# Kernel optimization log

Measured on AMD Instinct MI355X. Metric: run time of the kernel, lower is better.

Reference implementation:

```python
import jax, jax.numpy as jnp
import numpy as np

B, L, D, H = 2, 2048, 1024, 16
DK = D // H


def setup_inputs() -> dict:
    key = jax.random.key(0)
    ks = jax.random.split(key, 11)
    s = 1.0 / np.sqrt(D)
    inp = {
        "context_sequence": jax.random.normal(ks[0], (B, L, D), jnp.float32),
        "value_sequence": jax.random.normal(ks[1], (B, L, D), jnp.float32),
        "mask": jnp.tril(jnp.ones((L, L), jnp.int32)),  # causal mask [L, L]
        "Wq": jax.random.normal(ks[2], (D, D), jnp.float32) * s,
        "bq": jax.random.normal(ks[3], (D,), jnp.float32) * s,
        "Wk": jax.random.normal(ks[4], (D, D), jnp.float32) * s,
        "bk": jax.random.normal(ks[5], (D,), jnp.float32) * s,
        "Wv": jax.random.normal(ks[6], (D, D), jnp.float32) * s,
        "bv": jax.random.normal(ks[7], (D,), jnp.float32) * s,
        "Wo": jax.random.normal(ks[8], (D, D), jnp.float32) * s,
        "bo": jax.random.normal(ks[9], (D,), jnp.float32) * s,
    }
    return inp


def reference(context_sequence, value_sequence, mask, Wq, bq, Wk, bk, Wv, bv, Wo, bo):
    orig_dtype = context_sequence.dtype
    # QKV projections; Q,K from context, V from value stream
    Q = (context_sequence @ Wq + bq).reshape(B, L, H, DK)
    K = (context_sequence @ Wk + bk).reshape(B, L, H, DK)
    V = (value_sequence @ Wv + bv).reshape(B, L, H, DK)
    # fp32 QK^T with 1/sqrt(d_k) scaling -> [B, H, L, L]
    scores = jnp.einsum("bqhd,bkhd->bhqk", Q.astype(jnp.float32), K.astype(jnp.float32)) / jnp.sqrt(
        jnp.asarray(DK, jnp.float32)
    )
    # dtype-dependent neg fill (fp32 -> -inf); causal rows always have >=1 valid entry
    neg_fill = jnp.asarray(-jnp.inf, jnp.float32)
    scores = jnp.where(mask[None, None, :, :] == 0, neg_fill, scores)
    scores = scores.astype(orig_dtype)
    attn = jax.nn.softmax(scores, axis=-1)
    # dropout is identity in eval mode
    out = jnp.einsum("bhqk,bkhd->bqhd", attn, V).reshape(B, L, D)
    return out @ Wo + bo
```

## Files before the change

### kernel.cpp

```cpp
#include <hip/hip_runtime.h>
#include <hip/hip_bf16.h>
#include <stdint.h>

#define B_   2
#define L_   2048
#define D_   1024
#define H_   16
#define DK_  64

typedef __attribute__((ext_vector_type(4))) float f32x4;
typedef __attribute__((ext_vector_type(8))) short short8;
typedef unsigned short ushort_t;

__device__ __forceinline__ ushort_t f2bf(float f) {
    union { float f; uint32_t u; } v; v.f = f;
    uint32_t r = v.u + 0x7FFFu + ((v.u >> 16) & 1u);
    return (ushort_t)(r >> 16);
}
__device__ __forceinline__ float bf2f(ushort_t u) {
    union { uint32_t u; float f; } v; v.u = (uint32_t)u << 16; return v.f;
}
__device__ __forceinline__ uint32_t pack_bf16_rne(float a, float b) {
    return (uint32_t)f2bf(a) | ((uint32_t)f2bf(b) << 16);
}

__device__ __forceinline__ void async_copy16(void* lds, const void* g) {
    __builtin_amdgcn_global_load_lds(
        (const __attribute__((address_space(1))) uint32_t*)g,
        (__attribute__((address_space(3))) uint32_t*)lds, 16, 0, 0);
}

__global__ void cast_f32_bf16(const float* __restrict__ s0, const float* __restrict__ s1,
                              ushort_t* __restrict__ d0, ushort_t* __restrict__ d1) {
    const float* s = blockIdx.z ? s1 : s0;
    ushort_t*    d = blockIdx.z ? d1 : d0;
    int i = (blockIdx.x * 256 + threadIdx.x) * 4;
    float4 v = *(const float4*)(s + i);
    ushort4 o;
    o.x = f2bf(v.x); o.y = f2bf(v.y); o.z = f2bf(v.z); o.w = f2bf(v.w);
    *(ushort4*)(d + i) = o;
}

__global__ void transpose_w(const float* __restrict__ w0, const float* __restrict__ w1,
                            const float* __restrict__ w2, const float* __restrict__ w3,
                            ushort_t* __restrict__ out) {
    __shared__ float tile[32][33];
    const float* w = (blockIdx.z == 0) ? w0 : (blockIdx.z == 1) ? w1 : (blockIdx.z == 2) ? w2 : w3;
    ushort_t* o = out + (size_t)blockIdx.z * D_ * D_;
    int tx = threadIdx.x, ty = threadIdx.y;
    int k0 = blockIdx.y * 32, d0 = blockIdx.x * 32;
#pragma unroll
    for (int i = 0; i < 4; i++)
        tile[ty + i * 8][tx] = w[(size_t)(k0 + ty + i * 8) * D_ + d0 + tx];
    __syncthreads();
#pragma unroll
    for (int i = 0; i < 4; i++)
        o[(size_t)(d0 + ty + i * 8) * D_ + k0 + tx] = f2bf(tile[tx][ty + i * 8]);
}

template <bool SWAP>
__device__ __forceinline__ void gemm_main(const ushort_t* __restrict__ A,
                                          const ushort_t* __restrict__ WT,
                                          char* smem, int m0, int n0, int tid,
                                          f32x4 (&acc)[4][4]) {
    const int wid = tid >> 6, lane = tid & 63;
    const int wm = (wid >> 1) * 64, wn = (wid & 1) * 64;
#pragma unroll
    for (int i = 0; i < 4; i++)
#pragma unroll
        for (int j = 0; j < 4; j++) { f32x4 z = {0.f, 0.f, 0.f, 0.f}; acc[i][j] = z; }

    auto stage = [&](int buf, int k0) {
        char* bA = smem + buf * 32768;
        char* bB = bA + 16384;
#pragma unroll
        for (int i = 0; i < 4; i++) {
            int flat = i * 256 + tid; int row = flat >> 3; int win = (flat & 7) * 16;
            const char* srcA = (const char*)A + ((size_t)(m0 + row) * D_ + k0) * 2 + (win ^ ((row & 7) << 4));
            async_copy16(bA + (i * 256 + wid * 64) * 16, srcA);
            const char* srcB = (const char*)WT + ((size_t)(n0 + row) * D_ + k0) * 2 + (win ^ ((row & 7) << 4));
            async_copy16(bB + (i * 256 + wid * 64) * 16, srcB);
        }
    };

    stage(0, 0);
    int cur = 0;
    for (int k0 = 0; k0 < D_; k0 += 64) {
        __syncthreads();
        if (k0 + 64 < D_) stage(cur ^ 1, k0 + 64);
        const char* bA = smem + cur * 32768;
        const char* bB = bA + 16384;
#pragma unroll
        for (int ks = 0; ks < 2; ks++) {
            short8 af[4], bf[4];
            int kb = ks * 64 + ((lane >> 4) << 4);
#pragma unroll
            for (int t = 0; t < 4; t++) {
                int ml = wm + t * 16 + (lane & 15);
                af[t] = *(const short8*)(bA + ml * 128 + (kb ^ ((ml & 7) << 4)));
                int nl = wn + t * 16 + (lane & 15);
                bf[t] = *(const short8*)(bB + nl * 128 + (kb ^ ((nl & 7) << 4)));
            }
#pragma unroll
            for (int mt = 0; mt < 4; mt++)
#pragma unroll
                for (int nt = 0; nt < 4; nt++)
                    acc[mt][nt] = SWAP
                        ? __builtin_amdgcn_mfma_f32_16x16x32_bf16(bf[nt], af[mt], acc[mt][nt], 0, 0, 0)
                        : __builtin_amdgcn_mfma_f32_16x16x32_bf16(af[mt], bf[nt], acc[mt][nt], 0, 0, 0);
        }
        cur ^= 1;
    }
}

#define QSCALE 0.18033688f

template <int Z>
__global__ __launch_bounds__(256, 2) void gemm_qkv_t(
    const ushort_t* __restrict__ A, const ushort_t* __restrict__ WT,
    const float* __restrict__ bias, ushort_t* __restrict__ outp) {
    __shared__ __align__(16) char smem[65536];
    const int tid = threadIdx.x, wid = tid >> 6, lane = tid & 63;
    const int lo = lane & 15, hi = lane >> 4;
    const int m0 = blockIdx.y * 128, n0 = blockIdx.x * 128;
    const int wm = (wid >> 1) * 64, wn = (wid & 1) * 64;
    f32x4 acc[4][4];
    gemm_main<(Z != 2)>(A, WT, smem, m0, n0, tid, acc);
    if (Z != 2) {
#pragma unroll
        for (int mt = 0; mt < 4; mt++)
#pragma unroll
            for (int nt = 0; nt < 4; nt++) {
                int m  = m0 + wm + mt * 16 + lo;
                int nb = n0 + wn + nt * 16 + 4 * hi;
                float4 b4 = *(const float4*)(bias + nb);
                float v0 = acc[mt][nt][0] + b4.x;
                float v1 = acc[mt][nt][1] + b4.y;
                float v2 = acc[mt][nt][2] + b4.z;
                float v3 = acc[mt][nt][3] + b4.w;
                if (Z == 0) { v0 *= QSCALE; v1 *= QSCALE; v2 *= QSCALE; v3 *= QSCALE; }
                int b = m >> 11, tok = m & 2047, h = nb >> 6, dk = nb & 63;
                uint2 w;
                w.x = pack_bf16_rne(v0, v1);
                w.y = pack_bf16_rne(v2, v3);
                *(uint2*)(outp + ((size_t)(b * H_ + h) * L_ + tok) * DK_ + dk) = w;
            }
    } else {
#pragma unroll
        for (int mt = 0; mt < 4; mt++)
#pragma unroll
            for (int nt = 0; nt < 4; nt++) {
                int n  = n0 + wn + nt * 16 + lo;
                int mb = m0 + wm + mt * 16 + 4 * hi;
                float bv_ = bias[n];
                int b = mb >> 11, tok = mb & 2047, h = n >> 6, dk = n & 63;
                uint2 w;
                w.x = pack_bf16_rne(acc[mt][nt][0] + bv_, acc[mt][nt][1] + bv_);
                w.y = pack_bf16_rne(acc[mt][nt][2] + bv_, acc[mt][nt][3] + bv_);
                *(uint2*)(outp + ((size_t)(b * H_ + h) * DK_ + dk) * L_ + tok) = w;
            }
    }
}

__global__ __launch_bounds__(256, 2) void gemm_out(
    const ushort_t* __restrict__ O, const ushort_t* __restrict__ WT,
    const float* __restrict__ bo, float* __restrict__ out) {
    __shared__ __align__(16) char smem[65536];
    const int tid = threadIdx.x, wid = tid >> 6, lane = tid & 63;
    const int lo = lane & 15, hi = lane >> 4;
    const int m0 = blockIdx.y * 128, n0 = blockIdx.x * 128;
    const int wm = (wid >> 1) * 64, wn = (wid & 1) * 64;
    f32x4 acc[4][4];
    gemm_main<true>(O, WT, smem, m0, n0, tid, acc);
#pragma unroll
    for (int mt = 0; mt < 4; mt++)
#pragma unroll
        for (int nt = 0; nt < 4; nt++) {
            int m  = m0 + wm + mt * 16 + lo;
            int nb = n0 + wn + nt * 16 + 4 * hi;
            float4 b4 = *(const float4*)(bo + nb);
            float4 o;
            o.x = acc[mt][nt][0] + b4.x;
            o.y = acc[mt][nt][1] + b4.y;
            o.z = acc[mt][nt][2] + b4.z;
            o.w = acc[mt][nt][3] + b4.w;
            *(float4*)(out + (size_t)m * D_ + nb) = o;
        }
}

__global__ __launch_bounds__(256, 2) void attn_kernel(
    const ushort_t* __restrict__ qws, const ushort_t* __restrict__ kws,
    const ushort_t* __restrict__ vtws, ushort_t* __restrict__ ows) {
    __shared__ __align__(16) char smem[37888];
    const int tid = threadIdx.x, wid = tid >> 6, lane = tid & 63;
    const int lo = lane & 15, hi = lane >> 4;
    const int bid = blockIdx.x;
    const int xcd = bid & 7, slot = bid >> 3;
    const int bh = xcd * 4 + (slot >> 4);
    const int pi = slot & 15;
    char*  Pw = smem + wid * 9216;
    float* lall = (float*)(smem + 36864);
    float* lw = lall + wid * 64;
    const int swz = (lo & 7) << 4;

    short8 ones;
#pragma unroll
    for (int i = 0; i < 8; i++) ones[i] = (short)0x3F80;
    const f32x4 minit = {-32.f, -32.f, -32.f, -32.f};

#pragma unroll 1
    for (int half = 0; half < 2; half++) {
        const int qtb = half ? (31 - pi) : pi;
        const int Q0 = qtb * 64;

        short8 qf[4][2];
#pragma unroll
        for (int qt = 0; qt < 4; qt++)
#pragma unroll
            for (int ks = 0; ks < 2; ks++)
                qf[qt][ks] = *(const short8*)(qws + (size_t)(bh * L_ + Q0 + qt * 16 + lo) * DK_ + ks * 32 + hi * 8);

        f32x4 oa[4][4];
        f32x4 lf4[4];
#pragma unroll
        for (int qt = 0; qt < 4; qt++) {
            f32x4 z = {0.f, 0.f, 0.f, 0.f};
            lf4[qt] = z;
#pragma unroll
            for (int ot = 0; ot < 4; ot++) oa[qt][ot] = z;
        }

        const int ntiles = qtb + 1;
#pragma unroll 1
        for (int t = wid; t < ntiles; t += 4) {
            const int k0 = t * 64;
            const bool diag = (t == qtb);
            short8 vf[4][2];
#pragma unroll
            for (int ot = 0; ot < 4; ot++)
#pragma unroll
                for (int ks = 0; ks < 2; ks++)
                    vf[ot][ks] = *(const short8*)(vtws + (size_t)(bh * DK_ + ot * 16 + lo) * L_ + k0 + ks * 32 + hi * 8);

#pragma unroll
            for (int kt = 0; kt < 4; kt++) {
                const ushort_t* krow = kws + (size_t)(bh * L_ + k0 + kt * 16 + lo) * DK_ + hi * 8;
                short8 kf0 = *(const short8*)(krow);
                short8 kf1 = *(const short8*)(krow + 32);
                const int kb = kt * 16 + 4 * hi;
#pragma unroll
                for (int qt = 0; qt < 4; qt++) {
                    f32x4 s = __builtin_amdgcn_mfma_f32_16x16x32_bf16(kf0, qf[qt][0], minit, 0, 0, 0);
                    s = __builtin_amdgcn_mfma_f32_16x16x32_bf16(kf1, qf[qt][1], s, 0, 0, 0);
                    float p0 = exp2f(s[0]);
                    float p1 = exp2f(s[1]);
                    float p2 = exp2f(s[2]);
                    float p3 = exp2f(s[3]);
                    if (diag) {
                        const int qg = qt * 16 + lo;
                        p0 = (kb > qg)     ? 0.f : p0;
                        p1 = (kb + 1 > qg) ? 0.f : p1;
                        p2 = (kb + 2 > qg) ? 0.f : p2;
                        p3 = (kb + 3 > qg) ? 0.f : p3;
                    }
                    uint2 w;
                    w.x = __builtin_amdgcn_perm(__float_as_uint(p1), __float_as_uint(p0), 0x07060302u);
                    w.y = __builtin_amdgcn_perm(__float_as_uint(p3), __float_as_uint(p2), 0x07060302u);
                    *(uint2*)(Pw + qt * 2048 + lo * 128 + ((kt * 32 + hi * 8) ^ swz)) = w;
                }
            }
#pragma unroll
            for (int qt = 0; qt < 4; qt++)
#pragma unroll
                for (int ks = 0; ks < 2; ks++) {
                    short8 pf = *(const short8*)(Pw + qt * 2048 + lo * 128 + ((ks * 64 + hi * 16) ^ swz));
                    lf4[qt] = __builtin_amdgcn_mfma_f32_16x16x32_bf16(pf, ones, lf4[qt], 0, 0, 0);
#pragma unroll
                    for (int ot = 0; ot < 4; ot++)
                        oa[qt][ot] = __builtin_amdgcn_mfma_f32_16x16x32_bf16(pf, vf[ot][ks], oa[qt][ot], 0, 0, 0);
                }
        }

#pragma unroll
        for (int qt = 0; qt < 4; qt++)
#pragma unroll
            for (int ot = 0; ot < 4; ot++)
#pragma unroll
                for (int r = 0; r < 4; r++)
                    *(ushort_t*)(Pw + (qt * 16 + 4 * hi + r) * 144 + (ot * 16 + lo) * 2) = f2bf(oa[qt][ot][r]);
        if (lo == 0) {
#pragma unroll
            for (int qt = 0; qt < 4; qt++)
                *(f32x4*)(lw + qt * 16 + 4 * hi) = lf4[qt];
        }
        __syncthreads();

        {
            const int q = tid >> 2, c = tid & 3;
            float acc[16];
#pragma unroll
            for (int j = 0; j < 16; j++) acc[j] = 0.f;
#pragma unroll
            for (int w = 0; w < 4; w++) {
                const char* base = smem + w * 9216 + q * 144 + c * 32;
                short8 a = *(const short8*)(base);
                short8 b = *(const short8*)(base + 16);
#pragma unroll
                for (int j = 0; j < 8; j++) acc[j]     += bf2f((ushort_t)a[j]);
#pragma unroll
                for (int j = 0; j < 8; j++) acc[8 + j] += bf2f((ushort_t)b[j]);
            }
            float ls = 0.f;
#pragma unroll
            for (int w = 0; w < 4; w++) ls += lall[w * 64 + q];
            float ri = 1.0f / ls;
            short8 o0, o1;
#pragma unroll
            for (int j = 0; j < 8; j++) o0[j] = (short)f2bf(acc[j] * ri);
#pragma unroll
            for (int j = 0; j < 8; j++) o1[j] = (short)f2bf(acc[8 + j] * ri);
            size_t ob = (size_t)((bh >> 4) * L_ + Q0 + q) * D_ + (bh & 15) * DK_ + c * 16;
            *(short8*)(ows + ob)     = o0;
            *(short8*)(ows + ob + 8) = o1;
        }
        __syncthreads();
    }
}

extern "C" void kernel_launch(void* const* d_in, const int* in_sizes, int n_in,
                              void* d_out, int out_size, void* d_ws, size_t ws_size,
                              hipStream_t stream) {
    (void)in_sizes; (void)n_in; (void)out_size; (void)ws_size;
    const float* ctx = (const float*)d_in[0];
    const float* val = (const float*)d_in[1];
    const float* Wq = (const float*)d_in[3];
    const float* bq = (const float*)d_in[4];
    const float* Wk = (const float*)d_in[5];
    const float* bk = (const float*)d_in[6];
    const float* Wv = (const float*)d_in[7];
    const float* bv = (const float*)d_in[8];
    const float* Wo = (const float*)d_in[9];
    const float* bo = (const float*)d_in[10];
    float* out = (float*)d_out;

    char* ws = (char*)d_ws;
    ushort_t* xc  = (ushort_t*)(ws);
    ushort_t* xv  = (ushort_t*)(ws + 8388608);
    ushort_t* wt  = (ushort_t*)(ws + 16777216);
    ushort_t* qws = (ushort_t*)(ws + 25165824);
    ushort_t* kws = (ushort_t*)(ws + 33554432);
    ushort_t* vtw = (ushort_t*)(ws + 41943040);

    cast_f32_bf16<<<dim3(4096, 1, 2), 256, 0, stream>>>(ctx, val, xc, xv);
    transpose_w<<<dim3(32, 32, 4), dim3(32, 8), 0, stream>>>(Wq, Wk, Wv, Wo, wt);
    gemm_qkv_t<0><<<dim3(8, 32), 256, 0, stream>>>(xc, wt,                       bq, qws);
    gemm_qkv_t<1><<<dim3(8, 32), 256, 0, stream>>>(xc, wt + (size_t)1 * D_ * D_, bk, kws);
    gemm_qkv_t<2><<<dim3(8, 32), 256, 0, stream>>>(xv, wt + (size_t)2 * D_ * D_, bv, vtw);
    attn_kernel<<<dim3(512), 256, 0, stream>>>(qws, kws, vtw, xc );
    gemm_out<<<dim3(8, 32), 256, 0, stream>>>(xc, wt + (size_t)3 * D_ * D_, bo, out);
}
```

Before: 126.8 us.

## Merge QKV GEMMs into one launch, widen output GEMM, double-buffer attention P

Combines the three QKV projection GEMMs into a single launch using blockIdx.z, so more blocks are resident at once and two launches' worth of overhead and tail effects go away. The output projection GEMM moves to 512-thread blocks with 8 waves per tile, raising per-CU parallelism. The attention kernel double-buffers its per-wave P scratch in LDS and raises wave priority around the PV MFMA section, to overlap softmax writes with matrix work. The larger LDS footprint in attention may reduce occupancy.

```diff
diff --git a/kernel.cpp b/kernel.cpp
--- a/kernel.cpp
+++ b/kernel.cpp
@@ -113,20 +113,80 @@
     }
 }
 
+__device__ __forceinline__ void gemm_main8(const ushort_t* __restrict__ A,
+                                           const ushort_t* __restrict__ WT,
+                                           char* smem, int m0, int n0, int tid,
+                                           f32x4 (&acc)[4][2]) {
+    const int wid = tid >> 6, lane = tid & 63;
+    const int wm = (wid >> 2) * 64, wn = (wid & 3) * 32;
+#pragma unroll
+    for (int i = 0; i < 4; i++)
+#pragma unroll
+        for (int j = 0; j < 2; j++) { f32x4 z = {0.f, 0.f, 0.f, 0.f}; acc[i][j] = z; }
+
+    auto stage = [&](int buf, int k0) {
+        char* bA = smem + buf * 32768;
+        char* bB = bA + 16384;
+#pragma unroll
+        for (int i = 0; i < 2; i++) {
+            int flat = i * 512 + tid; int row = flat >> 3; int win = (flat & 7) * 16;
+            const char* srcA = (const char*)A + ((size_t)(m0 + row) * D_ + k0) * 2 + (win ^ ((row & 7) << 4));
+            async_copy16(bA + (i * 512 + wid * 64) * 16, srcA);
+            const char* srcB = (const char*)WT + ((size_t)(n0 + row) * D_ + k0) * 2 + (win ^ ((row & 7) << 4));
+            async_copy16(bB + (i * 512 + wid * 64) * 16, srcB);
+        }
+    };
+
+    stage(0, 0);
+    int cur = 0;
+    for (int k0 = 0; k0 < D_; k0 += 64) {
+        __syncthreads();
+        if (k0 + 64 < D_) stage(cur ^ 1, k0 + 64);
+        const char* bA = smem + cur * 32768;
+        const char* bB = bA + 16384;
+#pragma unroll
+        for (int ks = 0; ks < 2; ks++) {
+            short8 af[4], bf[2];
+            int kb = ks * 64 + ((lane >> 4) << 4);
+#pragma unroll
+            for (int t = 0; t < 4; t++) {
+                int ml = wm + t * 16 + (lane & 15);
+                af[t] = *(const short8*)(bA + ml * 128 + (kb ^ ((ml & 7) << 4)));
+            }
+#pragma unroll
+            for (int t = 0; t < 2; t++) {
+                int nl = wn + t * 16 + (lane & 15);
+                bf[t] = *(const short8*)(bB + nl * 128 + (kb ^ ((nl & 7) << 4)));
+            }
+#pragma unroll
+            for (int mt = 0; mt < 4; mt++)
+#pragma unroll
+                for (int nt = 0; nt < 2; nt++)
+                    acc[mt][nt] = __builtin_amdgcn_mfma_f32_16x16x32_bf16(bf[nt], af[mt], acc[mt][nt], 0, 0, 0);
+        }
+        cur ^= 1;
+    }
+}
+
 #define QSCALE 0.18033688f
 
-template <int Z>
-__global__ __launch_bounds__(256, 2) void gemm_qkv_t(
-    const ushort_t* __restrict__ A, const ushort_t* __restrict__ WT,
-    const float* __restrict__ bias, ushort_t* __restrict__ outp) {
+__global__ __launch_bounds__(256, 2) void gemm_qkv(
+    const ushort_t* __restrict__ Xc, const ushort_t* __restrict__ Xv,
+    const ushort_t* __restrict__ WT0,
+    const float* __restrict__ bq, const float* __restrict__ bk, const float* __restrict__ bv,
+    ushort_t* __restrict__ qw, ushort_t* __restrict__ kw, ushort_t* __restrict__ vtw) {
     __shared__ __align__(16) char smem[65536];
+    const int z = blockIdx.z;
+    const ushort_t* A  = (z == 2) ? Xv : Xc;
+    const ushort_t* WT = WT0 + (size_t)z * D_ * D_;
+    const float* bias  = (z == 0) ? bq : (z == 1) ? bk : bv;
     const int tid = threadIdx.x, wid = tid >> 6, lane = tid & 63;
     const int lo = lane & 15, hi = lane >> 4;
     const int m0 = blockIdx.y * 128, n0 = blockIdx.x * 128;
     const int wm = (wid >> 1) * 64, wn = (wid & 1) * 64;
     f32x4 acc[4][4];
-    gemm_main<(Z != 2)>(A, WT, smem, m0, n0, tid, acc);
-    if (Z != 2) {
+    if (z != 2) {
+        gemm_main<true>(A, WT, smem, m0, n0, tid, acc);
 #pragma unroll
         for (int mt = 0; mt < 4; mt++)
 #pragma unroll
@@ -138,14 +198,16 @@
                 float v1 = acc[mt][nt][1] + b4.y;
                 float v2 = acc[mt][nt][2] + b4.z;
                 float v3 = acc[mt][nt][3] + b4.w;
-                if (Z == 0) { v0 *= QSCALE; v1 *= QSCALE; v2 *= QSCALE; v3 *= QSCALE; }
+                if (z == 0) { v0 *= QSCALE; v1 *= QSCALE; v2 *= QSCALE; v3 *= QSCALE; }
                 int b = m >> 11, tok = m & 2047, h = nb >> 6, dk = nb & 63;
                 uint2 w;
                 w.x = pack_bf16_rne(v0, v1);
                 w.y = pack_bf16_rne(v2, v3);
+                ushort_t* outp = (z == 0) ? qw : kw;
                 *(uint2*)(outp + ((size_t)(b * H_ + h) * L_ + tok) * DK_ + dk) = w;
             }
     } else {
+        gemm_main<false>(A, WT, smem, m0, n0, tid, acc);
 #pragma unroll
         for (int mt = 0; mt < 4; mt++)
 #pragma unroll
@@ -157,25 +219,25 @@
                 uint2 w;
                 w.x = pack_bf16_rne(acc[mt][nt][0] + bv_, acc[mt][nt][1] + bv_);
                 w.y = pack_bf16_rne(acc[mt][nt][2] + bv_, acc[mt][nt][3] + bv_);
-                *(uint2*)(outp + ((size_t)(b * H_ + h) * DK_ + dk) * L_ + tok) = w;
+                *(uint2*)(vtw + ((size_t)(b * H_ + h) * DK_ + dk) * L_ + tok) = w;
             }
     }
 }
 
-__global__ __launch_bounds__(256, 2) void gemm_out(
+__global__ __launch_bounds__(512, 2) void gemm_out(
     const ushort_t* __restrict__ O, const ushort_t* __restrict__ WT,
     const float* __restrict__ bo, float* __restrict__ out) {
     __shared__ __align__(16) char smem[65536];
     const int tid = threadIdx.x, wid = tid >> 6, lane = tid & 63;
     const int lo = lane & 15, hi = lane >> 4;
     const int m0 = blockIdx.y * 128, n0 = blockIdx.x * 128;
-    const int wm = (wid >> 1) * 64, wn = (wid & 1) * 64;
-    f32x4 acc[4][4];
-    gemm_main<true>(O, WT, smem, m0, n0, tid, acc);
+    const int wm = (wid >> 2) * 64, wn = (wid & 3) * 32;
+    f32x4 acc[4][2];
+    gemm_main8(O, WT, smem, m0, n0, tid, acc);
 #pragma unroll
     for (int mt = 0; mt < 4; mt++)
 #pragma unroll
-        for (int nt = 0; nt < 4; nt++) {
+        for (int nt = 0; nt < 2; nt++) {
             int m  = m0 + wm + mt * 16 + lo;
             int nb = n0 + wn + nt * 16 + 4 * hi;
             float4 b4 = *(const float4*)(bo + nb);
@@ -191,15 +253,16 @@
 __global__ __launch_bounds__(256, 2) void attn_kernel(
     const ushort_t* __restrict__ qws, const ushort_t* __restrict__ kws,
     const ushort_t* __restrict__ vtws, ushort_t* __restrict__ ows) {
-    __shared__ __align__(16) char smem[37888];
+    __shared__ __align__(16) char smem[66560];
     const int tid = threadIdx.x, wid = tid >> 6, lane = tid & 63;
     const int lo = lane & 15, hi = lane >> 4;
     const int bid = blockIdx.x;
     const int xcd = bid & 7, slot = bid >> 3;
     const int bh = xcd * 4 + (slot >> 4);
     const int pi = slot & 15;
-    char*  Pw = smem + wid * 9216;
-    float* lall = (float*)(smem + 36864);
+    char* P0 = smem + wid * 16384;
+    char* P1 = P0 + 8192;
+    float* lall = (float*)(smem + 65536);
     float* lw = lall + wid * 64;
     const int swz = (lo & 7) << 4;
 
@@ -212,6 +275,7 @@
     for (int half = 0; half < 2; half++) {
         const int qtb = half ? (31 - pi) : pi;
         const int Q0 = qtb * 64;
+        const int ntiles = qtb + 1;
 
         short8 qf[4][2];
 #pragma unroll
@@ -230,18 +294,15 @@
             for (int ot = 0; ot < 4; ot++) oa[qt][ot] = z;
         }
 
-        const int ntiles = qtb + 1;
-#pragma unroll 1
-        for (int t = wid; t < ntiles; t += 4) {
+        auto TILE = [&](int t, char* Pb) {
             const int k0 = t * 64;
-            const bool diag = (t == qtb);
+            const bool diag = (t == ntiles - 1) && (ntiles - 1 == qtb);
             short8 vf[4][2];
 #pragma unroll
             for (int ot = 0; ot < 4; ot++)
 #pragma unroll
                 for (int ks = 0; ks < 2; ks++)
                     vf[ot][ks] = *(const short8*)(vtws + (size_t)(bh * DK_ + ot * 16 + lo) * L_ + k0 + ks * 32 + hi * 8);
-
 #pragma unroll
             for (int kt = 0; kt < 4; kt++) {
                 const ushort_t* krow = kws + (size_t)(bh * L_ + k0 + kt * 16 + lo) * DK_ + hi * 8;
@@ -266,20 +327,30 @@
                     uint2 w;
                     w.x = __builtin_amdgcn_perm(__float_as_uint(p1), __float_as_uint(p0), 0x07060302u);
                     w.y = __builtin_amdgcn_perm(__float_as_uint(p3), __float_as_uint(p2), 0x07060302u);
-                    *(uint2*)(Pw + qt * 2048 + lo * 128 + ((kt * 32 + hi * 8) ^ swz)) = w;
+                    *(uint2*)(Pb + qt * 2048 + lo * 128 + ((kt * 32 + hi * 8) ^ swz)) = w;
                 }
             }
+            __builtin_amdgcn_s_setprio(1);
 #pragma unroll
             for (int qt = 0; qt < 4; qt++)
 #pragma unroll
                 for (int ks = 0; ks < 2; ks++) {
-                    short8 pf = *(const short8*)(Pw + qt * 2048 + lo * 128 + ((ks * 64 + hi * 16) ^ swz));
+                    short8 pf = *(const short8*)(Pb + qt * 2048 + lo * 128 + ((ks * 64 + hi * 16) ^ swz));
                     lf4[qt] = __builtin_amdgcn_mfma_f32_16x16x32_bf16(pf, ones, lf4[qt], 0, 0, 0);
 #pragma unroll
                     for (int ot = 0; ot < 4; ot++)
                         oa[qt][ot] = __builtin_amdgcn_mfma_f32_16x16x32_bf16(pf, vf[ot][ks], oa[qt][ot], 0, 0, 0);
                 }
-        }
+            __builtin_amdgcn_s_setprio(0);
+        };
+
+        int t = wid;
+#pragma unroll 1
+        for (; t + 4 < ntiles; t += 8) {
+            TILE(t, P0);
+            TILE(t + 4, P1);
+        }
+        if (t < ntiles) TILE(t, P0);
 
 #pragma unroll
         for (int qt = 0; qt < 4; qt++)
@@ -287,7 +358,7 @@
             for (int ot = 0; ot < 4; ot++)
 #pragma unroll
                 for (int r = 0; r < 4; r++)
-                    *(ushort_t*)(Pw + (qt * 16 + 4 * hi + r) * 144 + (ot * 16 + lo) * 2) = f2bf(oa[qt][ot][r]);
+                    *(ushort_t*)(P0 + (qt * 16 + 4 * hi + r) * 144 + (ot * 16 + lo) * 2) = f2bf(oa[qt][ot][r]);
         if (lo == 0) {
 #pragma unroll
             for (int qt = 0; qt < 4; qt++)
@@ -302,7 +373,7 @@
             for (int j = 0; j < 16; j++) acc[j] = 0.f;
 #pragma unroll
             for (int w = 0; w < 4; w++) {
-                const char* base = smem + w * 9216 + q * 144 + c * 32;
+                const char* base = smem + w * 16384 + q * 144 + c * 32;
                 short8 a = *(const short8*)(base);
                 short8 b = *(const short8*)(base + 16);
 #pragma unroll
@@ -353,9 +424,7 @@
 
     cast_f32_bf16<<<dim3(4096, 1, 2), 256, 0, stream>>>(ctx, val, xc, xv);
     transpose_w<<<dim3(32, 32, 4), dim3(32, 8), 0, stream>>>(Wq, Wk, Wv, Wo, wt);
-    gemm_qkv_t<0><<<dim3(8, 32), 256, 0, stream>>>(xc, wt,                       bq, qws);
-    gemm_qkv_t<1><<<dim3(8, 32), 256, 0, stream>>>(xc, wt + (size_t)1 * D_ * D_, bk, kws);
-    gemm_qkv_t<2><<<dim3(8, 32), 256, 0, stream>>>(xv, wt + (size_t)2 * D_ * D_, bv, vtw);
+    gemm_qkv<<<dim3(8, 32, 3), 256, 0, stream>>>(xc, xv, wt, bq, bk, bv, qws, kws, vtw);
     attn_kernel<<<dim3(512), 256, 0, stream>>>(qws, kws, vtw, xc );
-    gemm_out<<<dim3(8, 32), 256, 0, stream>>>(xc, wt + (size_t)3 * D_ * D_, bo, out);
-}
+    gemm_out<<<dim3(8, 32), 512, 0, stream>>>(xc, wt + (size_t)3 * D_ * D_, bo, out);
+}
```

After: 116.6 us. 8.0% less time.
